# Kernel optimization log

Measured on AMD Instinct MI355X. Metric: run time of the kernel, lower is better.

Reference implementation:

```python
import jax, jax.numpy as jnp
import numpy as np

B, S, HID, NH, HD = 2, 2048, 768, 12, 64
WINDOW = 128           # ModernBERT local attention window
ROPE_THETA = 10000.0   # local_rope_theta (layer_index=0 -> is_local_attention=True)


def _rotate_half(x):
    x1, x2 = jnp.split(x, 2, axis=-1)
    return jnp.concatenate([-x2, x1], axis=-1)


def setup_inputs() -> dict:
    key = jax.random.key(0)
    k1, k2, k3 = jax.random.split(key, 3)
    hidden_embed = jax.random.normal(k1, (B, S, HID), dtype=jnp.float32)
    Wq = jax.random.normal(k2, (HID, HID), dtype=jnp.float32) * (HID ** -0.5)
    Wo = jax.random.normal(k3, (HID, HID), dtype=jnp.float32) * (HID ** -0.5)
    position_index = jnp.arange(S, dtype=jnp.int32).reshape(1, S)
    # sliding-window additive mask: 0 inside window, -inf outside
    i = jnp.arange(S)
    dist = jnp.abs(i[:, None] - i[None, :])
    local_attention_mask = jnp.where(dist <= WINDOW // 2, 0.0, -jnp.inf).astype(jnp.float32)[None, None]
    global_attention_mask = jnp.zeros((1, 1, S, S), dtype=jnp.float32)
    return {
        "hidden_embed": hidden_embed,
        "Wq": Wq,
        "Wo": Wo,
        "local_attention_mask": local_attention_mask,
        "global_attention_mask": global_attention_mask,
        "position_index": position_index,
    }


def reference(hidden_embed, Wq, Wo, local_attention_mask, global_attention_mask, position_index):
    # q projection; NOTE: source has k = q.view(...), v = q.view(...) -> k and v ARE q
    q = hidden_embed @ Wq.T                                  # [B,S,HID]
    q = q.reshape(B, S, NH, HD).transpose(0, 2, 1, 3)        # [B,NH,S,HD]

    # RoPE
    inv_freq = 1.0 / (ROPE_THETA ** (jnp.arange(0, HD, 2, dtype=jnp.float32) / HD))  # [HD/2]
    pos = position_index.reshape(-1).astype(jnp.float32)     # [S]
    freqs = pos[:, None] * inv_freq[None, :]                 # [S,HD/2]
    emb = jnp.concatenate([freqs, freqs], axis=-1)           # [S,HD]
    cos, sin = jnp.cos(emb), jnp.sin(emb)
    q_rot = q * cos + _rotate_half(q) * sin                  # [B,NH,S,HD]
    k_rot = q_rot                                            # k == q before rope -> same after rope
    v = q                                                    # v == q (no rope on v)

    # masked SDPA (local layer -> local sliding-window mask)
    scale = jnp.asarray(HD, jnp.float32) ** -0.5
    scores = jnp.einsum('bhtd,bhsd->bhts', q_rot, k_rot) * scale + local_attention_mask
    attn = jax.nn.softmax(scores, axis=-1)                   # [B,NH,S,S]
    out = jnp.einsum('bhts,bhsd->bhtd', attn, v)             # [B,NH,S,HD]
    out = out.transpose(0, 2, 1, 3).reshape(B, S, HID)
    return out @ Wo.T
```

## Files before the change

kernel.cpp:

```cpp
#include <hip/hip_runtime.h>
#include <hip/hip_bf16.h>
#include <math.h>
#include <stdint.h>

#define B_    2
#define S_    2048
#define HID_  768
#define NH_   12
#define HD_   64
#define NROWS (B_ * S_)
#define N_HID_ELEM (NROWS * HID_)
#define N_W_ELEM   (HID_ * HID_)

#define KW   224
#define KSTR 232

typedef __bf16 bf16x8 __attribute__((ext_vector_type(8)));
typedef float  floatx4 __attribute__((ext_vector_type(4)));

__global__ void convert_inputs_kernel(const float* __restrict__ src_hidden,
                                      const float* __restrict__ src_w1,
                                      const float* __restrict__ src_w2,
                                      __hip_bfloat16* __restrict__ Hb,
                                      __hip_bfloat16* __restrict__ Wqb,
                                      __hip_bfloat16* __restrict__ Wob)
{
    int i = blockIdx.x * blockDim.x + threadIdx.x;
    const float* src;
    __hip_bfloat16* dst;
    int off;
    const int NH4 = N_HID_ELEM / 4, NW4 = N_W_ELEM / 4;
    if (i < NH4)           { src = src_hidden; dst = Hb;  off = i; }
    else if (i < NH4+NW4)  { src = src_w1;     dst = Wqb; off = i - NH4; }
    else if (i < NH4+2*NW4){ src = src_w2;     dst = Wob; off = i - NH4 - NW4; }
    else return;
    float4 v = reinterpret_cast<const float4*>(src)[off];
    __hip_bfloat16 o[4] = { __float2bfloat16(v.x), __float2bfloat16(v.y),
                            __float2bfloat16(v.z), __float2bfloat16(v.w) };
    *reinterpret_cast<uint64_t*>(dst + 4 * (size_t)off) = *reinterpret_cast<uint64_t*>(o);
}

__device__ __forceinline__ void gload_lds16(const __hip_bfloat16* g, __hip_bfloat16* l)
{
    __builtin_amdgcn_global_load_lds(
        (const __attribute__((address_space(1))) void*)g,
        (__attribute__((address_space(3))) void*)l, 16, 0, 0);
}

template<int ROPE>
__global__ __launch_bounds__(512) void gemm64k2(
    const __hip_bfloat16* __restrict__ A,
    const __hip_bfloat16* __restrict__ W,
    __hip_bfloat16* __restrict__ C,
    __hip_bfloat16* __restrict__ C2,
    float* __restrict__ Cf,
    const int* __restrict__ pos_idx,
    int M, int N, int K)
{
    __shared__ __align__(16) __hip_bfloat16 Ald[2][2][2][64][32];
    __shared__ __align__(16) __hip_bfloat16 Wld[2][2][2][64][32];

    const int tid  = threadIdx.x;
    const int kg   = tid >> 8;
    const int wv4  = (tid >> 6) & 3;
    const int lane = tid & 63;
    const int l16  = lane & 15;
    const int quad = lane >> 4;
    const int m0 = blockIdx.x * 64;
    const int n0 = blockIdx.y * 64;

    const int c   = wv4 * 64 + lane;
    const int sr  = c >> 2;
    const int sc8 = (c & 3) * 8;
    const int kbase = kg * 384;

    const __hip_bfloat16* gA = A + (size_t)(m0 + sr) * K + kbase + sc8;
    const __hip_bfloat16* gW = W + (size_t)(n0 + sr) * K + kbase + sc8;

    floatx4 acc[4] = {};
    const int ra = wv4 * 16 + l16;

    gload_lds16(gA,      &Ald[kg][0][0][wv4 * 16][0]);
    gload_lds16(gA + 32, &Ald[kg][0][1][wv4 * 16][0]);
    gload_lds16(gW,      &Wld[kg][0][0][wv4 * 16][0]);
    gload_lds16(gW + 32, &Wld[kg][0][1][wv4 * 16][0]);

#pragma unroll
    for (int it = 0; it < 6; ++it) {
        const int cur = it & 1;
        __syncthreads();
        if (it + 1 < 6) {
            const int nb = (it + 1) & 1;
            const int ko = (it + 1) * 64;
            gload_lds16(gA + ko,      &Ald[kg][nb][0][wv4 * 16][0]);
            gload_lds16(gA + ko + 32, &Ald[kg][nb][1][wv4 * 16][0]);
            gload_lds16(gW + ko,      &Wld[kg][nb][0][wv4 * 16][0]);
            gload_lds16(gW + ko + 32, &Wld[kg][nb][1][wv4 * 16][0]);
        }
#pragma unroll
        for (int ks = 0; ks < 2; ++ks) {
            bf16x8 a = *reinterpret_cast<const bf16x8*>(&Ald[kg][cur][ks][ra][quad * 8]);
#pragma unroll
            for (int u = 0; u < 4; ++u) {
                bf16x8 w = *reinterpret_cast<const bf16x8*>(
                    &Wld[kg][cur][ks][u * 16 + l16][quad * 8]);
                acc[u] = __builtin_amdgcn_mfma_f32_16x16x32_bf16(a, w, acc[u], 0, 0, 0);
            }
        }
    }

    __syncthreads();
    float* Red = reinterpret_cast<float*>(&Ald[0][0][0][0][0]);
    if (kg == 1) {
#pragma unroll
        for (int u = 0; u < 4; ++u)
#pragma unroll
            for (int r = 0; r < 4; ++r)
                Red[(wv4 * 16 + quad * 4 + r) * 68 + u * 16 + l16] = acc[u][r];
    }
    __syncthreads();
    if (kg == 1) return;
#pragma unroll
    for (int u = 0; u < 4; ++u)
#pragma unroll
        for (int r = 0; r < 4; ++r)
            acc[u][r] += Red[(wv4 * 16 + quad * 4 + r) * 68 + u * 16 + l16];

    if (ROPE) {
#pragma unroll
        for (int r = 0; r < 4; ++r) {
            int m = m0 + wv4 * 16 + quad * 4 + r;
            int s = m & (S_ - 1);
            float pos = (float)pos_idx[s];
#pragma unroll
            for (int u = 0; u < 2; ++u) {
                float f = (float)(u * 16 + l16);
                float inv = exp2f(f * (-0.41524101186092024f));
                float sn, cs;
                sincosf(pos * inv, &sn, &cs);
                float q0 = acc[u][r];
                float q1 = acc[u + 2][r];
                size_t base = (size_t)m * HID_ + n0 + u * 16 + l16;
                C [base]      = __float2bfloat16(q0);
                C [base + 32] = __float2bfloat16(q1);
                C2[base]      = __float2bfloat16(q0 * cs - q1 * sn);
                C2[base + 32] = __float2bfloat16(q1 * cs + q0 * sn);
            }
        }
    } else {
#pragma unroll
        for (int u = 0; u < 4; ++u)
#pragma unroll
            for (int r = 0; r < 4; ++r) {
                int row = m0 + wv4 * 16 + quad * 4 + r;
                int col = n0 + u * 16 + l16;
                Cf[(size_t)row * N + col] = acc[u][r];
            }
    }
}

__global__ __launch_bounds__(256) void attn_kernel(
    const __hip_bfloat16* __restrict__ Q,
    const __hip_bfloat16* __restrict__ Qr,
    __hip_bfloat16* __restrict__ O)
{
    __shared__ __align__(16) __hip_bfloat16 Vt[64][KSTR];
    __shared__ __align__(16) __hip_bfloat16 Pl[64][KSTR];

    const int bh = blockIdx.y;
    const int b  = bh / NH_;
    const int h  = bh % NH_;
    const int i0 = blockIdx.x * 64;
    const int tid = threadIdx.x;

    for (int idx = tid; idx < KW * 8; idx += 256) {
        int w  = idx >> 3;
        int d8 = (idx & 7) * 8;
        int j  = i0 - 64 + w;
        int jc = min(max(j, 0), S_ - 1);
        bf16x8 v = *reinterpret_cast<const bf16x8*>(
            Q + ((size_t)(b * S_ + jc)) * HID_ + h * HD_ + d8);
        const __hip_bfloat16* ve = reinterpret_cast<const __hip_bfloat16*>(&v);
#pragma unroll
        for (int e = 0; e < 8; ++e) Vt[d8 + e][w] = ve[e];
    }
    __syncthreads();

    const int wv   = tid >> 6;
    const int lane = tid & 63;
    const int l16  = lane & 15;
    const int quad = lane >> 4;

    floatx4 sc[10] = {};
    const __hip_bfloat16* qrow =
        Qr + ((size_t)(b * S_ + i0 + wv * 16 + l16)) * HID_ + h * HD_ + quad * 8;
#pragma unroll
    for (int ks = 0; ks < 2; ++ks) {
        bf16x8 a = *reinterpret_cast<const bf16x8*>(qrow + ks * 32);
#pragma unroll
        for (int t = 0; t < 10; ++t) {
            int j = i0 - 64 + (wv + t) * 16 + l16;
            int jc = min(max(j, 0), S_ - 1);
            bf16x8 bfr = *reinterpret_cast<const bf16x8*>(
                Qr + ((size_t)(b * S_ + jc)) * HID_ + h * HD_ + ks * 32 + quad * 8);
            sc[t] = __builtin_amdgcn_mfma_f32_16x16x32_bf16(a, bfr, sc[t], 0, 0, 0);
        }
    }

    const float scale = 0.125f;
    float denom[4];
#pragma unroll
    for (int r = 0; r < 4; ++r) {
        const int R = wv * 16 + quad * 4 + r;
        float xv[10];
        float mx = -3.0e38f;
#pragma unroll
        for (int t = 0; t < 10; ++t) {
            int w = (wv + t) * 16 + l16;
            int j = i0 - 64 + w;
            bool valid = (w >= R) && (w <= R + 128) && (j >= 0) && (j < S_);
            float x = valid ? sc[t][r] * scale : -1.0e30f;
            xv[t] = x;
            mx = fmaxf(mx, x);
        }
#pragma unroll
        for (int msk = 1; msk < 16; msk <<= 1) mx = fmaxf(mx, __shfl_xor(mx, msk, 64));
        float sum = 0.f;
#pragma unroll
        for (int t = 0; t < 10; ++t) {
            float p = __expf(xv[t] - mx);
            sum += p;
            Pl[R][(wv + t) * 16 + l16] = __float2bfloat16(p);
        }
#pragma unroll
        for (int msk = 1; msk < 16; msk <<= 1) sum += __shfl_xor(sum, msk, 64);
        denom[r] = sum;
    }
    __syncthreads();

    floatx4 oacc[4] = {};
#pragma unroll
    for (int c = 0; c < 5; ++c) {
        const int base = wv * 16 + c * 32;
        bf16x8 a = *reinterpret_cast<const bf16x8*>(&Pl[wv * 16 + l16][base + quad * 8]);
#pragma unroll
        for (int u = 0; u < 4; ++u) {
            bf16x8 bfr = *reinterpret_cast<const bf16x8*>(&Vt[u * 16 + l16][base + quad * 8]);
            oacc[u] = __builtin_amdgcn_mfma_f32_16x16x32_bf16(a, bfr, oacc[u], 0, 0, 0);
        }
    }

    __syncthreads();
    float* Of = reinterpret_cast<float*>(&Pl[0][0]);
#pragma unroll
    for (int u = 0; u < 4; ++u)
#pragma unroll
        for (int r = 0; r < 4; ++r)
            Of[(wv * 16 + quad * 4 + r) * 68 + u * 16 + l16] = oacc[u][r] / denom[r];
    __syncthreads();
    {
        int row = tid >> 2;
        int seg = (tid & 3) * 16;
        __hip_bfloat16 ob[16];
#pragma unroll
        for (int e = 0; e < 16; ++e)
            ob[e] = __float2bfloat16(Of[row * 68 + seg + e]);
        __hip_bfloat16* dst = O + ((size_t)(b * S_ + i0 + row)) * HID_ + h * HD_ + seg;
        *reinterpret_cast<bf16x8*>(dst)     = *reinterpret_cast<bf16x8*>(ob);
        *reinterpret_cast<bf16x8*>(dst + 8) = *reinterpret_cast<bf16x8*>(ob + 8);
    }
}

extern "C" void kernel_launch(void* const* d_in, const int* in_sizes, int n_in,
                              void* d_out, int out_size, void* d_ws, size_t ws_size,
                              hipStream_t stream)
{
    int ih = -1, iw1 = -1, iw2 = -1, ip = -1;
    for (int i = 0; i < n_in; ++i) {
        int s = in_sizes[i];
        if      (s == N_HID_ELEM && ih < 0) ih = i;
        else if (s == N_W_ELEM)  { if (iw1 < 0) iw1 = i; else if (iw2 < 0) iw2 = i; }
        else if (s == S_ && ip < 0) ip = i;
    }
    if (ih < 0)  ih = 0;
    if (iw1 < 0) iw1 = 1;
    if (iw2 < 0) iw2 = 2;
    if (ip < 0)  ip = 5;

    const float* hidden = (const float*)d_in[ih];
    const float* w1     = (const float*)d_in[iw1];
    const float* w2     = (const float*)d_in[iw2];
    const int*   pos    = (const int*)d_in[ip];

    __hip_bfloat16* Hb  = (__hip_bfloat16*)d_ws;
    __hip_bfloat16* Wqb = Hb  + N_HID_ELEM;
    __hip_bfloat16* Wob = Wqb + N_W_ELEM;
    __hip_bfloat16* Q   = Wob + N_W_ELEM;
    __hip_bfloat16* Qr  = Q   + N_HID_ELEM;
    __hip_bfloat16* AO  = Hb;

    int conv4 = (N_HID_ELEM + 2 * N_W_ELEM) / 4;
    convert_inputs_kernel<<<(conv4 + 255) / 256, 256, 0, stream>>>(
        hidden, w1, w2, Hb, Wqb, Wob);

    dim3 gblk(NROWS / 64, HID_ / 64);

    gemm64k2<1><<<gblk, 512, 0, stream>>>(Hb, Wqb, Q, Qr, nullptr, pos,
                                          NROWS, HID_, HID_);

    attn_kernel<<<dim3(S_ / 64, B_ * NH_), 256, 0, stream>>>(Q, Qr, AO);

    gemm64k2<0><<<gblk, 512, 0, stream>>>(AO, Wob, nullptr, nullptr, (float*)d_out,
                                          nullptr, NROWS, HID_, HID_);
}
```

Before: 143.6 us.

## Fuse all stages into one cooperative persistent kernel with grid syncs

Replaces the four separate launches (convert, Q-projection GEMM with RoPE, windowed attention, output GEMM) with one persistent cooperative kernel. The stages are separated by grid.sync and blocks loop over tiles. This is meant to remove launch gaps and tail effects between kernels. The GEMM also loses its split-K double-buffered pipeline: it becomes a single-buffered 256-thread loop that syncs twice per K step, which may lower GEMM throughput. A fallback path keeps separate launches if the cooperative launch fails.

```diff
diff --git a/kernel.cpp b/kernel.cpp
--- a/kernel.cpp
+++ b/kernel.cpp
@@ -1,7 +1,10 @@
 #include <hip/hip_runtime.h>
+#include <hip/hip_cooperative_groups.h>
 #include <hip/hip_bf16.h>
 #include <math.h>
 #include <stdint.h>
+
+namespace cg = cooperative_groups;
 
 #define B_    2
 #define S_    2048
@@ -14,31 +17,11 @@
 
 #define KW   224
 #define KSTR 232
+#define MAX_BLKS 512
+#define NTHR  256
 
 typedef __bf16 bf16x8 __attribute__((ext_vector_type(8)));
 typedef float  floatx4 __attribute__((ext_vector_type(4)));
-
-__global__ void convert_inputs_kernel(const float* __restrict__ src_hidden,
-                                      const float* __restrict__ src_w1,
-                                      const float* __restrict__ src_w2,
-                                      __hip_bfloat16* __restrict__ Hb,
-                                      __hip_bfloat16* __restrict__ Wqb,
-                                      __hip_bfloat16* __restrict__ Wob)
-{
-    int i = blockIdx.x * blockDim.x + threadIdx.x;
-    const float* src;
-    __hip_bfloat16* dst;
-    int off;
-    const int NH4 = N_HID_ELEM / 4, NW4 = N_W_ELEM / 4;
-    if (i < NH4)           { src = src_hidden; dst = Hb;  off = i; }
-    else if (i < NH4+NW4)  { src = src_w1;     dst = Wqb; off = i - NH4; }
-    else if (i < NH4+2*NW4){ src = src_w2;     dst = Wob; off = i - NH4 - NW4; }
-    else return;
-    float4 v = reinterpret_cast<const float4*>(src)[off];
-    __hip_bfloat16 o[4] = { __float2bfloat16(v.x), __float2bfloat16(v.y),
-                            __float2bfloat16(v.z), __float2bfloat16(v.w) };
-    *reinterpret_cast<uint64_t*>(dst + 4 * (size_t)off) = *reinterpret_cast<uint64_t*>(o);
-}
 
 __device__ __forceinline__ void gload_lds16(const __hip_bfloat16* g, __hip_bfloat16* l)
 {
@@ -47,89 +30,82 @@
         (__attribute__((address_space(3))) void*)l, 16, 0, 0);
 }
 
+__device__ __forceinline__ void convert_body(
+    int start, int stride,
+    const float* __restrict__ hidden, const float* __restrict__ w1,
+    const float* __restrict__ w2,
+    __hip_bfloat16* __restrict__ Hb, __hip_bfloat16* __restrict__ Wqb,
+    __hip_bfloat16* __restrict__ Wob)
+{
+    const int NH4 = N_HID_ELEM / 4, NW4 = N_W_ELEM / 4;
+    const int TOT4 = NH4 + 2 * NW4;
+    for (int i = start; i < TOT4; i += stride) {
+        const float* src;
+        __hip_bfloat16* dst;
+        int off;
+        if (i < NH4)            { src = hidden; dst = Hb;  off = i; }
+        else if (i < NH4 + NW4) { src = w1;     dst = Wqb; off = i - NH4; }
+        else                    { src = w2;     dst = Wob; off = i - NH4 - NW4; }
+        float4 v = reinterpret_cast<const float4*>(src)[off];
+        __hip_bfloat16 o[4] = { __float2bfloat16(v.x), __float2bfloat16(v.y),
+                                __float2bfloat16(v.z), __float2bfloat16(v.w) };
+        *reinterpret_cast<uint64_t*>(dst + 4 * (size_t)off) =
+            *reinterpret_cast<uint64_t*>(o);
+    }
+}
+
 template<int ROPE>
-__global__ __launch_bounds__(512) void gemm64k2(
+__device__ __forceinline__ void gemm_tile(
     const __hip_bfloat16* __restrict__ A,
     const __hip_bfloat16* __restrict__ W,
-    __hip_bfloat16* __restrict__ C,
-    __hip_bfloat16* __restrict__ C2,
-    float* __restrict__ Cf,
-    const int* __restrict__ pos_idx,
-    int M, int N, int K)
-{
-    __shared__ __align__(16) __hip_bfloat16 Ald[2][2][2][64][32];
-    __shared__ __align__(16) __hip_bfloat16 Wld[2][2][2][64][32];
-
+    __hip_bfloat16* __restrict__ C, __hip_bfloat16* __restrict__ C2,
+    float* __restrict__ Cf, const int* __restrict__ pos_idx,
+    int m0, int n0, int K, int N,
+    __hip_bfloat16* __restrict__ smA, __hip_bfloat16* __restrict__ smW)
+{
     const int tid  = threadIdx.x;
-    const int kg   = tid >> 8;
-    const int wv4  = (tid >> 6) & 3;
+    const int wv   = tid >> 6;
     const int lane = tid & 63;
     const int l16  = lane & 15;
     const int quad = lane >> 4;
-    const int m0 = blockIdx.x * 64;
-    const int n0 = blockIdx.y * 64;
-
-    const int c   = wv4 * 64 + lane;
+
+    const int c   = wv * 64 + lane;
     const int sr  = c >> 2;
     const int sc8 = (c & 3) * 8;
-    const int kbase = kg * 384;
-
-    const __hip_bfloat16* gA = A + (size_t)(m0 + sr) * K + kbase + sc8;
-    const __hip_bfloat16* gW = W + (size_t)(n0 + sr) * K + kbase + sc8;
+
+    const __hip_bfloat16* gA = A + (size_t)(m0 + sr) * K + sc8;
+    const __hip_bfloat16* gW = W + (size_t)(n0 + sr) * K + sc8;
+    __hip_bfloat16* lA0 = smA + (wv * 16) * 32;
+    __hip_bfloat16* lA1 = smA + 2048 + (wv * 16) * 32;
+    __hip_bfloat16* lW0 = smW + (wv * 16) * 32;
+    __hip_bfloat16* lW1 = smW + 2048 + (wv * 16) * 32;
 
     floatx4 acc[4] = {};
-    const int ra = wv4 * 16 + l16;
-
-    gload_lds16(gA,      &Ald[kg][0][0][wv4 * 16][0]);
-    gload_lds16(gA + 32, &Ald[kg][0][1][wv4 * 16][0]);
-    gload_lds16(gW,      &Wld[kg][0][0][wv4 * 16][0]);
-    gload_lds16(gW + 32, &Wld[kg][0][1][wv4 * 16][0]);
-
-#pragma unroll
-    for (int it = 0; it < 6; ++it) {
-        const int cur = it & 1;
+    const int ra = wv * 16 + l16;
+
+    for (int k0 = 0; k0 < K; k0 += 64) {
+        gload_lds16(gA + k0,      lA0);
+        gload_lds16(gA + k0 + 32, lA1);
+        gload_lds16(gW + k0,      lW0);
+        gload_lds16(gW + k0 + 32, lW1);
         __syncthreads();
-        if (it + 1 < 6) {
-            const int nb = (it + 1) & 1;
-            const int ko = (it + 1) * 64;
-            gload_lds16(gA + ko,      &Ald[kg][nb][0][wv4 * 16][0]);
-            gload_lds16(gA + ko + 32, &Ald[kg][nb][1][wv4 * 16][0]);
-            gload_lds16(gW + ko,      &Wld[kg][nb][0][wv4 * 16][0]);
-            gload_lds16(gW + ko + 32, &Wld[kg][nb][1][wv4 * 16][0]);
-        }
 #pragma unroll
         for (int ks = 0; ks < 2; ++ks) {
-            bf16x8 a = *reinterpret_cast<const bf16x8*>(&Ald[kg][cur][ks][ra][quad * 8]);
+            bf16x8 a = *reinterpret_cast<const bf16x8*>(&smA[ks * 2048 + ra * 32 + quad * 8]);
 #pragma unroll
             for (int u = 0; u < 4; ++u) {
                 bf16x8 w = *reinterpret_cast<const bf16x8*>(
-                    &Wld[kg][cur][ks][u * 16 + l16][quad * 8]);
+                    &smW[ks * 2048 + (u * 16 + l16) * 32 + quad * 8]);
                 acc[u] = __builtin_amdgcn_mfma_f32_16x16x32_bf16(a, w, acc[u], 0, 0, 0);
             }
         }
-    }
-
-    __syncthreads();
-    float* Red = reinterpret_cast<float*>(&Ald[0][0][0][0][0]);
-    if (kg == 1) {
-#pragma unroll
-        for (int u = 0; u < 4; ++u)
-#pragma unroll
-            for (int r = 0; r < 4; ++r)
-                Red[(wv4 * 16 + quad * 4 + r) * 68 + u * 16 + l16] = acc[u][r];
-    }
-    __syncthreads();
-    if (kg == 1) return;
-#pragma unroll
-    for (int u = 0; u < 4; ++u)
-#pragma unroll
-        for (int r = 0; r < 4; ++r)
-            acc[u][r] += Red[(wv4 * 16 + quad * 4 + r) * 68 + u * 16 + l16];
+        __syncthreads();
+    }
 
     if (ROPE) {
 #pragma unroll
         for (int r = 0; r < 4; ++r) {
-            int m = m0 + wv4 * 16 + quad * 4 + r;
+            int m = m0 + wv * 16 + quad * 4 + r;
             int s = m & (S_ - 1);
             float pos = (float)pos_idx[s];
 #pragma unroll
@@ -152,28 +128,23 @@
         for (int u = 0; u < 4; ++u)
 #pragma unroll
             for (int r = 0; r < 4; ++r) {
-                int row = m0 + wv4 * 16 + quad * 4 + r;
+                int row = m0 + wv * 16 + quad * 4 + r;
                 int col = n0 + u * 16 + l16;
                 Cf[(size_t)row * N + col] = acc[u][r];
             }
     }
 }
 
-__global__ __launch_bounds__(256) void attn_kernel(
+__device__ __forceinline__ void attn_tile(
     const __hip_bfloat16* __restrict__ Q,
     const __hip_bfloat16* __restrict__ Qr,
-    __hip_bfloat16* __restrict__ O)
-{
-    __shared__ __align__(16) __hip_bfloat16 Vt[64][KSTR];
-    __shared__ __align__(16) __hip_bfloat16 Pl[64][KSTR];
-
-    const int bh = blockIdx.y;
-    const int b  = bh / NH_;
-    const int h  = bh % NH_;
-    const int i0 = blockIdx.x * 64;
+    __hip_bfloat16* __restrict__ O,
+    int b, int h, int i0,
+    __hip_bfloat16* __restrict__ VtB, __hip_bfloat16* __restrict__ PlB)
+{
     const int tid = threadIdx.x;
 
-    for (int idx = tid; idx < KW * 8; idx += 256) {
+    for (int idx = tid; idx < KW * 8; idx += NTHR) {
         int w  = idx >> 3;
         int d8 = (idx & 7) * 8;
         int j  = i0 - 64 + w;
@@ -182,7 +153,7 @@
             Q + ((size_t)(b * S_ + jc)) * HID_ + h * HD_ + d8);
         const __hip_bfloat16* ve = reinterpret_cast<const __hip_bfloat16*>(&v);
 #pragma unroll
-        for (int e = 0; e < 8; ++e) Vt[d8 + e][w] = ve[e];
+        for (int e = 0; e < 8; ++e) VtB[(d8 + e) * KSTR + w] = ve[e];
     }
     __syncthreads();
 
@@ -230,7 +201,7 @@
         for (int t = 0; t < 10; ++t) {
             float p = __expf(xv[t] - mx);
             sum += p;
-            Pl[R][(wv + t) * 16 + l16] = __float2bfloat16(p);
+            PlB[R * KSTR + (wv + t) * 16 + l16] = __float2bfloat16(p);
         }
 #pragma unroll
         for (int msk = 1; msk < 16; msk <<= 1) sum += __shfl_xor(sum, msk, 64);
@@ -242,16 +213,16 @@
 #pragma unroll
     for (int c = 0; c < 5; ++c) {
         const int base = wv * 16 + c * 32;
-        bf16x8 a = *reinterpret_cast<const bf16x8*>(&Pl[wv * 16 + l16][base + quad * 8]);
+        bf16x8 a = *reinterpret_cast<const bf16x8*>(&PlB[(wv * 16 + l16) * KSTR + base + quad * 8]);
 #pragma unroll
         for (int u = 0; u < 4; ++u) {
-            bf16x8 bfr = *reinterpret_cast<const bf16x8*>(&Vt[u * 16 + l16][base + quad * 8]);
+            bf16x8 bfr = *reinterpret_cast<const bf16x8*>(&VtB[(u * 16 + l16) * KSTR + base + quad * 8]);
             oacc[u] = __builtin_amdgcn_mfma_f32_16x16x32_bf16(a, bfr, oacc[u], 0, 0, 0);
         }
     }
 
     __syncthreads();
-    float* Of = reinterpret_cast<float*>(&Pl[0][0]);
+    float* Of = reinterpret_cast<float*>(PlB);
 #pragma unroll
     for (int u = 0; u < 4; ++u)
 #pragma unroll
@@ -269,6 +240,93 @@
         *reinterpret_cast<bf16x8*>(dst)     = *reinterpret_cast<bf16x8*>(ob);
         *reinterpret_cast<bf16x8*>(dst + 8) = *reinterpret_cast<bf16x8*>(ob + 8);
     }
+    __syncthreads();
+}
+
+__global__ __launch_bounds__(NTHR) void fused_all(
+    const float* __restrict__ hidden, const float* __restrict__ w1,
+    const float* __restrict__ w2, const int* __restrict__ pos,
+    __hip_bfloat16* __restrict__ Hb, __hip_bfloat16* __restrict__ Wqb,
+    __hip_bfloat16* __restrict__ Wob, __hip_bfloat16* __restrict__ Q,
+    __hip_bfloat16* __restrict__ Qr, float* __restrict__ out)
+{
+    __shared__ __align__(16) unsigned char smraw[2 * 64 * KSTR * 2];
+    __hip_bfloat16* sm0 = reinterpret_cast<__hip_bfloat16*>(smraw);
+
+    cg::grid_group grid = cg::this_grid();
+    const int bid   = blockIdx.x;
+    const int nblk  = gridDim.x;
+    const int tid   = threadIdx.x;
+
+    convert_body(bid * NTHR + tid, nblk * NTHR, hidden, w1, w2, Hb, Wqb, Wob);
+    __threadfence();
+    grid.sync();
+
+    {
+        __hip_bfloat16* smA = sm0;
+        __hip_bfloat16* smW = sm0 + 4096;
+        for (int job = bid; job < 64 * 12; job += nblk) {
+            int m0 = (job & 63) * 64;
+            int n0 = (job >> 6) * 64;
+            gemm_tile<1>(Hb, Wqb, Q, Qr, nullptr, pos, m0, n0, HID_, HID_, smA, smW);
+        }
+    }
+    __threadfence();
+    grid.sync();
+
+    {
+        __hip_bfloat16* VtB = sm0;
+        __hip_bfloat16* PlB = sm0 + 64 * KSTR;
+        for (int job = bid; job < 32 * B_ * NH_; job += nblk) {
+            int i0 = (job & 31) * 64;
+            int bh = job >> 5;
+            attn_tile(Q, Qr, Hb, bh / NH_, bh % NH_, i0, VtB, PlB);
+        }
+    }
+    __threadfence();
+    grid.sync();
+
+    {
+        __hip_bfloat16* smA = sm0;
+        __hip_bfloat16* smW = sm0 + 4096;
+        for (int job = bid; job < 64 * 12; job += nblk) {
+            int m0 = (job & 63) * 64;
+            int n0 = (job >> 6) * 64;
+            gemm_tile<0>(Hb, Wob, nullptr, nullptr, out, nullptr, m0, n0, HID_, HID_, smA, smW);
+        }
+    }
+}
+
+__global__ __launch_bounds__(NTHR) void convert_sa(
+    const float* __restrict__ hidden, const float* __restrict__ w1,
+    const float* __restrict__ w2,
+    __hip_bfloat16* __restrict__ Hb, __hip_bfloat16* __restrict__ Wqb,
+    __hip_bfloat16* __restrict__ Wob)
+{
+    convert_body(blockIdx.x * NTHR + threadIdx.x, gridDim.x * NTHR,
+                 hidden, w1, w2, Hb, Wqb, Wob);
+}
+
+template<int ROPE>
+__global__ __launch_bounds__(NTHR) void gemm_sa(
+    const __hip_bfloat16* __restrict__ A, const __hip_bfloat16* __restrict__ W,
+    __hip_bfloat16* __restrict__ C, __hip_bfloat16* __restrict__ C2,
+    float* __restrict__ Cf, const int* __restrict__ pos_idx)
+{
+    __shared__ __align__(16) __hip_bfloat16 smA[4096];
+    __shared__ __align__(16) __hip_bfloat16 smW[4096];
+    gemm_tile<ROPE>(A, W, C, C2, Cf, pos_idx,
+                    blockIdx.x * 64, blockIdx.y * 64, HID_, HID_, smA, smW);
+}
+
+__global__ __launch_bounds__(NTHR) void attn_sa(
+    const __hip_bfloat16* __restrict__ Q, const __hip_bfloat16* __restrict__ Qr,
+    __hip_bfloat16* __restrict__ O)
+{
+    __shared__ __align__(16) __hip_bfloat16 VtB[64 * KSTR];
+    __shared__ __align__(16) __hip_bfloat16 PlB[64 * KSTR];
+    int bh = blockIdx.y;
+    attn_tile(Q, Qr, O, bh / NH_, bh % NH_, blockIdx.x * 64, VtB, PlB);
 }
 
 extern "C" void kernel_launch(void* const* d_in, const int* in_sizes, int n_in,
@@ -297,19 +355,31 @@
     __hip_bfloat16* Wob = Wqb + N_W_ELEM;
     __hip_bfloat16* Q   = Wob + N_W_ELEM;
     __hip_bfloat16* Qr  = Q   + N_HID_ELEM;
-    __hip_bfloat16* AO  = Hb;
-
-    int conv4 = (N_HID_ELEM + 2 * N_W_ELEM) / 4;
-    convert_inputs_kernel<<<(conv4 + 255) / 256, 256, 0, stream>>>(
-        hidden, w1, w2, Hb, Wqb, Wob);
-
-    dim3 gblk(NROWS / 64, HID_ / 64);
-
-    gemm64k2<1><<<gblk, 512, 0, stream>>>(Hb, Wqb, Q, Qr, nullptr, pos,
-                                          NROWS, HID_, HID_);
-
-    attn_kernel<<<dim3(S_ / 64, B_ * NH_), 256, 0, stream>>>(Q, Qr, AO);
-
-    gemm64k2<0><<<gblk, 512, 0, stream>>>(AO, Wob, nullptr, nullptr, (float*)d_out,
-                                          nullptr, NROWS, HID_, HID_);
-}
+    float* out          = (float*)d_out;
+
+    bool launched = false;
+    int maxPerCU = 0;
+    hipError_t oe = hipOccupancyMaxActiveBlocksPerMultiprocessor(
+        &maxPerCU, (const void*)fused_all, NTHR, 0);
+    if (oe == hipSuccess && maxPerCU > 0) {
+        int nblk = maxPerCU * 256;
+        if (nblk > MAX_BLKS) nblk = MAX_BLKS;
+        void* args[] = { (void*)&hidden, (void*)&w1, (void*)&w2, (void*)&pos,
+                         (void*)&Hb, (void*)&Wqb, (void*)&Wob, (void*)&Q,
+                         (void*)&Qr, (void*)&out };
+        hipError_t le = hipLaunchCooperativeKernel(
+            (const void*)fused_all, dim3(nblk), dim3(NTHR), args, 0, stream);
+        launched = (le == hipSuccess);
+    }
+
+    if (!launched) {
+        const int NH4 = N_HID_ELEM / 4, NW4 = N_W_ELEM / 4;
+        int conv4 = NH4 + 2 * NW4;
+        convert_sa<<<(conv4 + NTHR - 1) / NTHR, NTHR, 0, stream>>>(
+            hidden, w1, w2, Hb, Wqb, Wob);
+        dim3 gblk(NROWS / 64, HID_ / 64);
+        gemm_sa<1><<<gblk, NTHR, 0, stream>>>(Hb, Wqb, Q, Qr, nullptr, pos);
+        attn_sa<<<dim3(S_ / 64, B_ * NH_), NTHR, 0, stream>>>(Q, Qr, Hb);
+        gemm_sa<0><<<gblk, NTHR, 0, stream>>>(Hb, Wob, nullptr, nullptr, out, nullptr);
+    }
+}
```

Result: slower. 363.6 us (+153.2%).

## Replace split-K double-buffered GEMM with smaller 32x64 single-buffer tiles

Applied to the files above, without the earlier changes.

Replaces the 512-thread split-K GEMM (two K halves, double-buffered LDS, cross-group reduction) with a 128-thread kernel that computes a 32x64 output tile over the full K in a simple load-sync-compute-sync loop. This doubles the number of blocks, removes the LDS reduction step, and shrinks LDS per block, which should raise occupancy. In exchange it gives up double buffering, so global-to-LDS loads no longer overlap with MFMA work, and each block issues fewer MFMAs per loaded weight tile.

```diff
diff --git a/kernel.cpp b/kernel.cpp
--- a/kernel.cpp
+++ b/kernel.cpp
@@ -48,7 +48,7 @@
 }
 
 template<int ROPE>
-__global__ __launch_bounds__(512) void gemm64k2(
+__global__ __launch_bounds__(128) void gemm32(
     const __hip_bfloat16* __restrict__ A,
     const __hip_bfloat16* __restrict__ W,
     __hip_bfloat16* __restrict__ C,
@@ -57,79 +57,62 @@
     const int* __restrict__ pos_idx,
     int M, int N, int K)
 {
-    __shared__ __align__(16) __hip_bfloat16 Ald[2][2][2][64][32];
-    __shared__ __align__(16) __hip_bfloat16 Wld[2][2][2][64][32];
+    __shared__ __align__(16) __hip_bfloat16 Ald[2][32][32];
+    __shared__ __align__(16) __hip_bfloat16 Wld[2][64][32];
 
     const int tid  = threadIdx.x;
-    const int kg   = tid >> 8;
-    const int wv4  = (tid >> 6) & 3;
+    const int wv   = tid >> 6;
     const int lane = tid & 63;
     const int l16  = lane & 15;
     const int quad = lane >> 4;
-    const int m0 = blockIdx.x * 64;
+    const int m0 = blockIdx.x * 32;
     const int n0 = blockIdx.y * 64;
 
-    const int c   = wv4 * 64 + lane;
-    const int sr  = c >> 2;
-    const int sc8 = (c & 3) * 8;
-    const int kbase = kg * 384;
-
-    const __hip_bfloat16* gA = A + (size_t)(m0 + sr) * K + kbase + sc8;
-    const __hip_bfloat16* gW = W + (size_t)(n0 + sr) * K + kbase + sc8;
+    const int sr  = tid >> 2;
+    const int sc8 = (tid & 3) * 8;
+
+    const __hip_bfloat16* gA0 = A + (size_t)(m0 + sr) * K + sc8;
+    const __hip_bfloat16* gA1 = A + (size_t)(m0 + sr) * K + 32 + sc8;
+    const __hip_bfloat16* gW0a = W + (size_t)(n0 + sr) * K + sc8;
+    const __hip_bfloat16* gW0b = W + (size_t)(n0 + 32 + sr) * K + sc8;
+    const __hip_bfloat16* gW1a = W + (size_t)(n0 + sr) * K + 32 + sc8;
+    const __hip_bfloat16* gW1b = W + (size_t)(n0 + 32 + sr) * K + 32 + sc8;
+
+    __hip_bfloat16* lA0  = &Ald[0][wv * 16][0];
+    __hip_bfloat16* lA1  = &Ald[1][wv * 16][0];
+    __hip_bfloat16* lW0a = &Wld[0][wv * 16][0];
+    __hip_bfloat16* lW0b = &Wld[0][32 + wv * 16][0];
+    __hip_bfloat16* lW1a = &Wld[1][wv * 16][0];
+    __hip_bfloat16* lW1b = &Wld[1][32 + wv * 16][0];
 
     floatx4 acc[4] = {};
-    const int ra = wv4 * 16 + l16;
-
-    gload_lds16(gA,      &Ald[kg][0][0][wv4 * 16][0]);
-    gload_lds16(gA + 32, &Ald[kg][0][1][wv4 * 16][0]);
-    gload_lds16(gW,      &Wld[kg][0][0][wv4 * 16][0]);
-    gload_lds16(gW + 32, &Wld[kg][0][1][wv4 * 16][0]);
-
-#pragma unroll
-    for (int it = 0; it < 6; ++it) {
-        const int cur = it & 1;
+    const int ra = wv * 16 + l16;
+
+    for (int k0 = 0; k0 < K; k0 += 64) {
+        gload_lds16(gA0  + k0, lA0);
+        gload_lds16(gA1  + k0, lA1);
+        gload_lds16(gW0a + k0, lW0a);
+        gload_lds16(gW0b + k0, lW0b);
+        gload_lds16(gW1a + k0, lW1a);
+        gload_lds16(gW1b + k0, lW1b);
         __syncthreads();
-        if (it + 1 < 6) {
-            const int nb = (it + 1) & 1;
-            const int ko = (it + 1) * 64;
-            gload_lds16(gA + ko,      &Ald[kg][nb][0][wv4 * 16][0]);
-            gload_lds16(gA + ko + 32, &Ald[kg][nb][1][wv4 * 16][0]);
-            gload_lds16(gW + ko,      &Wld[kg][nb][0][wv4 * 16][0]);
-            gload_lds16(gW + ko + 32, &Wld[kg][nb][1][wv4 * 16][0]);
-        }
+
 #pragma unroll
         for (int ks = 0; ks < 2; ++ks) {
-            bf16x8 a = *reinterpret_cast<const bf16x8*>(&Ald[kg][cur][ks][ra][quad * 8]);
+            bf16x8 a = *reinterpret_cast<const bf16x8*>(&Ald[ks][ra][quad * 8]);
 #pragma unroll
             for (int u = 0; u < 4; ++u) {
-                bf16x8 w = *reinterpret_cast<const bf16x8*>(
-                    &Wld[kg][cur][ks][u * 16 + l16][quad * 8]);
+                bf16x8 w = *reinterpret_cast<const bf16x8*>(&Wld[ks][u * 16 + l16][quad * 8]);
                 acc[u] = __builtin_amdgcn_mfma_f32_16x16x32_bf16(a, w, acc[u], 0, 0, 0);
             }
         }
-    }
-
-    __syncthreads();
-    float* Red = reinterpret_cast<float*>(&Ald[0][0][0][0][0]);
-    if (kg == 1) {
-#pragma unroll
-        for (int u = 0; u < 4; ++u)
-#pragma unroll
-            for (int r = 0; r < 4; ++r)
-                Red[(wv4 * 16 + quad * 4 + r) * 68 + u * 16 + l16] = acc[u][r];
-    }
-    __syncthreads();
-    if (kg == 1) return;
-#pragma unroll
-    for (int u = 0; u < 4; ++u)
-#pragma unroll
-        for (int r = 0; r < 4; ++r)
-            acc[u][r] += Red[(wv4 * 16 + quad * 4 + r) * 68 + u * 16 + l16];
+        __syncthreads();
+    }
 
     if (ROPE) {
 #pragma unroll
         for (int r = 0; r < 4; ++r) {
-            int m = m0 + wv4 * 16 + quad * 4 + r;
+            int m = m0 + wv * 16 + quad * 4 + r;
             int s = m & (S_ - 1);
             float pos = (float)pos_idx[s];
 #pragma unroll
@@ -152,7 +135,7 @@
         for (int u = 0; u < 4; ++u)
 #pragma unroll
             for (int r = 0; r < 4; ++r) {
-                int row = m0 + wv4 * 16 + quad * 4 + r;
+                int row = m0 + wv * 16 + quad * 4 + r;
                 int col = n0 + u * 16 + l16;
                 Cf[(size_t)row * N + col] = acc[u][r];
             }
@@ -303,13 +286,13 @@
     convert_inputs_kernel<<<(conv4 + 255) / 256, 256, 0, stream>>>(
         hidden, w1, w2, Hb, Wqb, Wob);
 
-    dim3 gblk(NROWS / 64, HID_ / 64);
-
-    gemm64k2<1><<<gblk, 512, 0, stream>>>(Hb, Wqb, Q, Qr, nullptr, pos,
-                                          NROWS, HID_, HID_);
+    dim3 gblk(NROWS / 32, HID_ / 64);
+
+    gemm32<1><<<gblk, 128, 0, stream>>>(Hb, Wqb, Q, Qr, nullptr, pos,
+                                        NROWS, HID_, HID_);
 
     attn_kernel<<<dim3(S_ / 64, B_ * NH_), 256, 0, stream>>>(Q, Qr, AO);
 
-    gemm64k2<0><<<gblk, 512, 0, stream>>>(AO, Wob, nullptr, nullptr, (float*)d_out,
-                                          nullptr, NROWS, HID_, HID_);
-}
+    gemm32<0><<<gblk, 128, 0, stream>>>(AO, Wob, nullptr, nullptr, (float*)d_out,
+                                        nullptr, NROWS, HID_, HID_);
+}
```

New measurement: 144.2 us. No clear change (+0.4%).
